# Kernel optimization log

Measured on AMD Instinct MI355X. Metric: run time of the kernel, lower is better.

## Reference

```python
import jax, jax.numpy as jnp
import numpy as np

B, S, L, D, H = 4, 4, 1024, 1024, 16  # batch, state_size, seq_len, d_model, num_heads
DEPTH = D // H
NEG = -1.0e9


def setup_inputs() -> dict:
    key = jax.random.key(0)
    ks = jax.random.split(key, 10)
    scale = 1.0 / np.sqrt(D)
    q = jax.random.normal(ks[0], (B, S, L, D), jnp.float32)
    k = jax.random.normal(ks[1], (B, S, L, D), jnp.float32)
    v = jax.random.normal(ks[2], (B, S, L, D), jnp.float32)
    mask = (jax.random.uniform(ks[3], (B, S, L, L)) < 0.1).astype(jnp.float32)
    wq = jax.random.normal(ks[4], (D, D), jnp.float32) * scale
    wk = jax.random.normal(ks[5], (D, D), jnp.float32) * scale
    wv = jax.random.normal(ks[6], (D, D), jnp.float32) * scale
    wo = jax.random.normal(ks[7], (D, D), jnp.float32) * scale
    bq = jnp.zeros((D,), jnp.float32)
    bk = jnp.zeros((D,), jnp.float32)
    bv = jnp.zeros((D,), jnp.float32)
    bo = jnp.zeros((D,), jnp.float32)
    return {"q": q, "k": k, "v": v, "mask": mask, "wq": wq, "bq": bq,
            "wk": wk, "bk": bk, "wv": wv, "bv": bv, "wo": wo, "bo": bo}


def _split_heads(x):
    # [B,S,L,D] -> [B,S,H,L,depth]
    b, s, l, _ = x.shape
    return x.reshape(b, s, l, H, DEPTH).transpose(0, 1, 3, 2, 4)


def reference(q, k, v, mask, wq, bq, wk, bk, wv, bv, wo, bo):
    qh = _split_heads(q @ wq + bq)
    kh = _split_heads(k @ wk + bk)
    vh = _split_heads(v @ wv + bv)
    # scaled dot-product attention, logits: [B,S,H,Lq,Lk]
    logits = jnp.einsum('bshqd,bshkd->bshqk', qh, kh) / jnp.sqrt(
        jnp.asarray(DEPTH, jnp.float32))
    logits = logits + mask[:, :, None, :, :] * NEG
    attn = jax.nn.softmax(logits, axis=-1)
    ctx = jnp.einsum('bshqk,bshkd->bshqd', attn, vh)
    # merge heads: [B,S,H,L,depth] -> [B,S,L,D]
    ctx = ctx.transpose(0, 1, 3, 2, 4).reshape(q.shape[0], q.shape[1], q.shape[2], D)
    out = ctx @ wo + bo
    attn_mean = attn.mean(axis=2)  # mean over heads -> [B,S,Lq,Lk]
    return out, attn_mean
```

## Files before the change

### kernel.cpp

```cpp
#include <hip/hip_runtime.h>

typedef _Float16 h16;
typedef _Float16 v8h __attribute__((ext_vector_type(8)));
typedef float    v4f __attribute__((ext_vector_type(4)));
typedef unsigned long long u64;

constexpr float SCALE = 0.125f;

#define MFMA16(a,b,c) __builtin_amdgcn_mfma_f32_16x16x32_f16((a),(b),(c),0,0,0)

__device__ __forceinline__ void gld16(const h16* g, const h16* l)
{
    __builtin_amdgcn_global_load_lds(
        (const __attribute__((address_space(1))) void*)g,
        (__attribute__((address_space(3))) void*)l, 16, 0, 0);
}

__global__ __launch_bounds__(256)
void cvt16(const float* __restrict__ x, h16* __restrict__ y)
{
    size_t i = ((size_t)blockIdx.x * 256 + threadIdx.x) * 4;
    float4 v = *(const float4*)(x + i);
    h16 o[4] = {(h16)v.x, (h16)v.y, (h16)v.z, (h16)v.w};
    *(uint2*)(y + i) = *(const uint2*)o;
}

__global__ __launch_bounds__(256)
void mkbits(const float* __restrict__ mask, u64* __restrict__ mb)
{
    size_t i = (size_t)blockIdx.x * 256 + threadIdx.x;
    float v = mask[i];
    u64 b = __ballot(v != 0.0f);
    if ((threadIdx.x & 63) == 0) mb[i >> 6] = b;
}

__global__ __launch_bounds__(256)
void wtrans(const float* __restrict__ W, h16* __restrict__ WT)
{
    __shared__ float Ts[64][65];
    const int tid = threadIdx.x;
    const int n0 = blockIdx.x * 64, k0 = blockIdx.y * 64;
    #pragma unroll
    for (int i = 0; i < 4; ++i) {
        int f = tid + i * 256; int r = f >> 4, c = (f & 15) * 4;
        float4 v = *(const float4*)(W + (size_t)(k0 + r) * 1024 + n0 + c);
        Ts[r][c] = v.x; Ts[r][c+1] = v.y; Ts[r][c+2] = v.z; Ts[r][c+3] = v.w;
    }
    __syncthreads();
    #pragma unroll
    for (int i = 0; i < 4; ++i) {
        int f = tid + i * 256; int r = f >> 4, c = (f & 15) * 4;
        h16 o[4];
        #pragma unroll
        for (int j = 0; j < 4; ++j) o[j] = (h16)Ts[c + j][r];
        *(uint2*)(WT + (size_t)(n0 + r) * 1024 + k0 + c) = *(const uint2*)o;
    }
}

__global__ __launch_bounds__(256)
void proj(const h16* __restrict__ A, const h16* __restrict__ BT,
          const float* __restrict__ bias, void* __restrict__ out, int mode)
{
    __shared__ h16 As[128 * 32];
    __shared__ h16 Bs[128 * 32];
    const int tid  = threadIdx.x;
    const int lane = tid & 63, wv = tid >> 6;
    const int quad = lane >> 4, l16 = lane & 15;
    const int m0 = blockIdx.y * 128, n0 = blockIdx.x * 128;
    const int wm = (wv & 1) * 64, wn = (wv >> 1) * 64;
    const int sr = wv * 16 + (lane >> 2);
    const int sc = (lane & 3) * 8;
    v4f acc[4][4] = {};
    for (int k0 = 0; k0 < 1024; k0 += 32) {
        #pragma unroll
        for (int i = 0; i < 2; ++i) {
            int r = i * 64 + sr;
            gld16(A  + (size_t)(m0 + r) * 1024 + k0 + sc, &As[i * 2048 + wv * 512]);
            gld16(BT + (size_t)(n0 + r) * 1024 + k0 + sc, &Bs[i * 2048 + wv * 512]);
        }
        __syncthreads();
        v8h af[4], bf[4];
        #pragma unroll
        for (int t = 0; t < 4; ++t) {
            af[t] = *(v8h*)&As[(wm + t*16 + l16) * 32 + quad * 8];
            bf[t] = *(v8h*)&Bs[(wn + t*16 + l16) * 32 + quad * 8];
        }
        #pragma unroll
        for (int mt = 0; mt < 4; ++mt)
            #pragma unroll
            for (int nt = 0; nt < 4; ++nt)
                acc[mt][nt] = MFMA16(af[mt], bf[nt], acc[mt][nt]);
        __syncthreads();
    }
    #pragma unroll
    for (int mt = 0; mt < 4; ++mt) {
        int mbase = m0 + wm + mt*16 + quad*4;
        #pragma unroll
        for (int nt = 0; nt < 4; ++nt) {
            int n = n0 + wn + nt*16 + l16;
            float bv = bias[n];
            #pragma unroll
            for (int r = 0; r < 4; ++r) {
                float y = acc[mt][nt][r] + bv;
                int mm = mbase + r;
                int bs = mm >> 10, l = mm & 1023, h = n >> 6, d = n & 63;
                if (mode <= 1)
                    ((h16*)out)[(((size_t)bs*16 + h) * 1024 + l) * 64 + d] = (h16)y;
                else if (mode == 2)
                    ((h16*)out)[(((size_t)bs*16 + h) * 64 + d) * 1024 + l] = (h16)y;
                else
                    ((float*)out)[(size_t)mm * 1024 + n] = y;
            }
        }
    }
}

__global__ __launch_bounds__(256)
void attn_ctx(const h16* __restrict__ qh, const h16* __restrict__ kh,
              const h16* __restrict__ vt, const u64* __restrict__ mbits,
              h16* __restrict__ ctx, float* __restrict__ Lst)
{
    __shared__ h16 Qs[128][72];
    __shared__ h16 Ks[64][72];
    __shared__ h16 Vs[64][72];
    __shared__ h16 Ps[128][72];
    const int tid  = threadIdx.x;
    const int lane = tid & 63, wv = tid >> 6;
    const int quad = lane >> 4, l16 = lane & 15;
    const int bsh = blockIdx.x, qb = blockIdx.y * 128;
    const int bs = bsh >> 4, h = bsh & 15;
    const int qw = wv * 32;
    #pragma unroll
    for (int i = 0; i < 4; ++i) {
        int f = tid + i * 256; int r = f >> 3, c = (f & 7) * 8;
        *(uint4*)&Qs[r][c] = *(const uint4*)(qh + ((size_t)bsh*1024 + qb + r) * 64 + c);
    }
    v4f accp[2][4] = {};
    float lsum[8] = {};
    for (int kt = 0; kt < 16; ++kt) {
        __syncthreads();
        #pragma unroll
        for (int i = 0; i < 2; ++i) {
            int f = tid + i * 256; int r = f >> 3, c = (f & 7) * 8;
            *(uint4*)&Ks[r][c] = *(const uint4*)(kh + ((size_t)bsh*1024 + kt*64 + r) * 64 + c);
            *(uint4*)&Vs[r][c] = *(const uint4*)(vt + ((size_t)bsh*64 + r) * 1024 + kt*64 + c);
        }
        __syncthreads();
        v4f s[2][4] = {};
        #pragma unroll
        for (int kc = 0; kc < 2; ++kc) {
            v8h aq[2], bk[4];
            aq[0] = *(v8h*)&Qs[qw      + l16][kc*32 + quad*8];
            aq[1] = *(v8h*)&Qs[qw + 16 + l16][kc*32 + quad*8];
            #pragma unroll
            for (int nt = 0; nt < 4; ++nt)
                bk[nt] = *(v8h*)&Ks[nt*16 + l16][kc*32 + quad*8];
            #pragma unroll
            for (int mt = 0; mt < 2; ++mt)
                #pragma unroll
                for (int nt = 0; nt < 4; ++nt)
                    s[mt][nt] = MFMA16(aq[mt], bk[nt], s[mt][nt]);
        }
        #pragma unroll
        for (int mt = 0; mt < 2; ++mt)
            #pragma unroll
            for (int r = 0; r < 4; ++r) {
                int ql = qw + mt*16 + quad*4 + r;
                u64 mrow = mbits[((size_t)bs*1024 + qb + ql) * 16 + kt];
                #pragma unroll
                for (int nt = 0; nt < 4; ++nt) {
                    int kl = nt*16 + l16;
                    float p = ((mrow >> kl) & 1ull) ? 0.0f
                                                    : __expf(s[mt][nt][r] * SCALE);
                    lsum[mt*4 + r] += p;
                    Ps[ql][kl] = (h16)p;
                }
            }
        __syncthreads();
        #pragma unroll
        for (int kc = 0; kc < 2; ++kc) {
            v8h ap[2], bv[4];
            ap[0] = *(v8h*)&Ps[qw      + l16][kc*32 + quad*8];
            ap[1] = *(v8h*)&Ps[qw + 16 + l16][kc*32 + quad*8];
            #pragma unroll
            for (int nt = 0; nt < 4; ++nt)
                bv[nt] = *(v8h*)&Vs[nt*16 + l16][kc*32 + quad*8];
            #pragma unroll
            for (int mt = 0; mt < 2; ++mt)
                #pragma unroll
                for (int nt = 0; nt < 4; ++nt)
                    accp[mt][nt] = MFMA16(ap[mt], bv[nt], accp[mt][nt]);
        }
    }
    #pragma unroll
    for (int j = 0; j < 8; ++j) {
        float v = lsum[j];
        #pragma unroll
        for (int o = 1; o < 16; o <<= 1) v += __shfl_xor(v, o);
        lsum[j] = v;
    }
    if (l16 == 0) {
        #pragma unroll
        for (int mt = 0; mt < 2; ++mt)
            #pragma unroll
            for (int r = 0; r < 4; ++r)
                Lst[(size_t)bsh*1024 + qb + qw + mt*16 + quad*4 + r] = lsum[mt*4 + r];
    }
    #pragma unroll
    for (int mt = 0; mt < 2; ++mt)
        #pragma unroll
        for (int nt = 0; nt < 4; ++nt) {
            int dep = nt*16 + l16;
            #pragma unroll
            for (int r = 0; r < 4; ++r) {
                int ql = qw + mt*16 + quad*4 + r;
                float y = accp[mt][nt][r] / lsum[mt*4 + r];
                ctx[((size_t)bs*1024 + qb + ql) * 1024 + h*64 + dep] = (h16)y;
            }
        }
}

__global__ __launch_bounds__(256)
void attn_mean_k(const h16* __restrict__ qh, const h16* __restrict__ kh,
                 const u64* __restrict__ mbits, const float* __restrict__ Lst,
                 float* __restrict__ am)
{
    __shared__ h16 Qs[128][72];
    __shared__ h16 Ks[64][72];
    const int tid  = threadIdx.x;
    const int lane = tid & 63, wv = tid >> 6;
    const int quad = lane >> 4, l16 = lane & 15;
    const int kt = blockIdx.x, qb = blockIdx.y * 128, bs = blockIdx.z;
    const int qw = wv * 32;
    u64 mrow[2][4];
    #pragma unroll
    for (int mt = 0; mt < 2; ++mt)
        #pragma unroll
        for (int r = 0; r < 4; ++r) {
            int ql = qw + mt*16 + quad*4 + r;
            mrow[mt][r] = mbits[((size_t)bs*1024 + qb + ql) * 16 + kt];
        }
    float acc[2][4][4] = {};
    for (int h = 0; h < 16; ++h) {
        const int bsh = bs * 16 + h;
        __syncthreads();
        #pragma unroll
        for (int i = 0; i < 4; ++i) {
            int f = tid + i * 256; int r = f >> 3, c = (f & 7) * 8;
            *(uint4*)&Qs[r][c] = *(const uint4*)(qh + ((size_t)bsh*1024 + qb + r) * 64 + c);
        }
        #pragma unroll
        for (int i = 0; i < 2; ++i) {
            int f = tid + i * 256; int r = f >> 3, c = (f & 7) * 8;
            *(uint4*)&Ks[r][c] = *(const uint4*)(kh + ((size_t)bsh*1024 + kt*64 + r) * 64 + c);
        }
        __syncthreads();
        v4f s[2][4] = {};
        #pragma unroll
        for (int kc = 0; kc < 2; ++kc) {
            v8h aq[2], bk[4];
            aq[0] = *(v8h*)&Qs[qw      + l16][kc*32 + quad*8];
            aq[1] = *(v8h*)&Qs[qw + 16 + l16][kc*32 + quad*8];
            #pragma unroll
            for (int nt = 0; nt < 4; ++nt)
                bk[nt] = *(v8h*)&Ks[nt*16 + l16][kc*32 + quad*8];
            #pragma unroll
            for (int mt = 0; mt < 2; ++mt)
                #pragma unroll
                for (int nt = 0; nt < 4; ++nt)
                    s[mt][nt] = MFMA16(aq[mt], bk[nt], s[mt][nt]);
        }
        float rl[8];
        #pragma unroll
        for (int mt = 0; mt < 2; ++mt)
            #pragma unroll
            for (int r = 0; r < 4; ++r)
                rl[mt*4+r] = 1.0f / Lst[(size_t)bsh*1024 + qb + qw + mt*16 + quad*4 + r];
        #pragma unroll
        for (int mt = 0; mt < 2; ++mt)
            #pragma unroll
            for (int nt = 0; nt < 4; ++nt) {
                int kl = nt*16 + l16;
                #pragma unroll
                for (int r = 0; r < 4; ++r) {
                    float e = ((mrow[mt][r] >> kl) & 1ull) ? 0.0f
                                                           : __expf(s[mt][nt][r] * SCALE);
                    acc[mt][nt][r] += e * rl[mt*4+r];
                }
            }
    }
    #pragma unroll
    for (int mt = 0; mt < 2; ++mt)
        #pragma unroll
        for (int nt = 0; nt < 4; ++nt)
            #pragma unroll
            for (int r = 0; r < 4; ++r) {
                int ql = qw + mt*16 + quad*4 + r;
                am[((size_t)bs*1024 + ql + qb) * 1024 + kt*64 + nt*16 + l16]
                    = acc[mt][nt][r] * 0.0625f;
            }
}

extern "C" void kernel_launch(void* const* d_in, const int* in_sizes, int n_in,
                              void* d_out, int out_size, void* d_ws, size_t ws_size,
                              hipStream_t stream)
{
    const float* q    = (const float*)d_in[0];
    const float* k    = (const float*)d_in[1];
    const float* v    = (const float*)d_in[2];
    const float* mask = (const float*)d_in[3];
    const float* wq   = (const float*)d_in[4];
    const float* bq   = (const float*)d_in[5];
    const float* wk   = (const float*)d_in[6];
    const float* bk   = (const float*)d_in[7];
    const float* wv   = (const float*)d_in[8];
    const float* bv   = (const float*)d_in[9];
    const float* wo   = (const float*)d_in[10];
    const float* bo   = (const float*)d_in[11];

    const size_t TEN = (size_t)16384 * 1024;
    char* w = (char*)d_ws;
    h16* qf  = (h16*)w;             w += TEN * 2;
    h16* kf  = (h16*)w;             w += TEN * 2;
    h16* vf  = (h16*)w;             w += TEN * 2;
    h16* wqT = (h16*)w;             w += (size_t)1024*1024*2;
    h16* wkT = (h16*)w;             w += (size_t)1024*1024*2;
    h16* wvT = (h16*)w;             w += (size_t)1024*1024*2;
    h16* woT = (h16*)w;             w += (size_t)1024*1024*2;
    h16* qhh = (h16*)w;             w += TEN * 2;
    h16* khh = (h16*)w;             w += TEN * 2;
    h16* vtt = (h16*)w;             w += TEN * 2;
    h16* ctx = (h16*)w;             w += TEN * 2;
    float* Lst = (float*)w;         w += (size_t)256 * 1024 * 4;
    u64* mbits = (u64*)w;

    float* out = (float*)d_out;
    float* am  = out + TEN;

    mkbits<<<65536, 256, 0, stream>>>(mask, mbits);
    cvt16<<<16384, 256, 0, stream>>>(q, qf);
    cvt16<<<16384, 256, 0, stream>>>(k, kf);
    cvt16<<<16384, 256, 0, stream>>>(v, vf);
    wtrans<<<dim3(16,16), 256, 0, stream>>>(wq, wqT);
    wtrans<<<dim3(16,16), 256, 0, stream>>>(wk, wkT);
    wtrans<<<dim3(16,16), 256, 0, stream>>>(wv, wvT);
    wtrans<<<dim3(16,16), 256, 0, stream>>>(wo, woT);
    proj<<<dim3(8,128), 256, 0, stream>>>(qf, wqT, bq, qhh, 0);
    proj<<<dim3(8,128), 256, 0, stream>>>(kf, wkT, bk, khh, 1);
    proj<<<dim3(8,128), 256, 0, stream>>>(vf, wvT, bv, vtt, 2);
    attn_ctx<<<dim3(256,8), 256, 0, stream>>>(qhh, khh, vtt, mbits, ctx, Lst);
    attn_mean_k<<<dim3(16,8,16), 256, 0, stream>>>(qhh, khh, mbits, Lst, am);
    proj<<<dim3(8,128), 256, 0, stream>>>(ctx, woT, bo, out, 3);
}
```

Measured before the change: 900.1 us.

## Fold softmax scale into Q, use exp2, MFMA row sums, register prefetch, block swizzle

```diff
diff --git a/kernel.cpp b/kernel.cpp
--- a/kernel.cpp
+++ b/kernel.cpp
@@ -5,9 +5,24 @@
 typedef float    v4f __attribute__((ext_vector_type(4)));
 typedef unsigned long long u64;
 
-constexpr float SCALE = 0.125f;
+constexpr float QPRESCALE = 0.18033688f;
 
 #define MFMA16(a,b,c) __builtin_amdgcn_mfma_f32_16x16x32_f16((a),(b),(c),0,0,0)
+
+__device__ __forceinline__ float fexp2(float x) {
+#if __has_builtin(__builtin_amdgcn_exp2f)
+    return __builtin_amdgcn_exp2f(x);
+#else
+    return __expf(x * 0.69314718056f);
+#endif
+}
+__device__ __forceinline__ float flog2(float x) {
+#if __has_builtin(__builtin_amdgcn_logf)
+    return __builtin_amdgcn_logf(x);
+#else
+    return __logf(x) * 1.44269504f;
+#endif
+}
 
 __device__ __forceinline__ void gld16(const h16* g, const h16* l)
 {
@@ -102,6 +117,7 @@
             #pragma unroll
             for (int r = 0; r < 4; ++r) {
                 float y = acc[mt][nt][r] + bv;
+                if (mode == 0) y *= QPRESCALE;
                 int mm = mbase + r;
                 int bs = mm >> 10, l = mm & 1023, h = n >> 6, d = n & 63;
                 if (mode <= 1)
@@ -115,35 +131,57 @@
     }
 }
 
-__global__ __launch_bounds__(256)
+__global__ __launch_bounds__(256, 3)
 void attn_ctx(const h16* __restrict__ qh, const h16* __restrict__ kh,
               const h16* __restrict__ vt, const u64* __restrict__ mbits,
               h16* __restrict__ ctx, float* __restrict__ Lst)
 {
-    __shared__ h16 Qs[128][72];
-    __shared__ h16 Ks[64][72];
-    __shared__ h16 Vs[64][72];
-    __shared__ h16 Ps[128][72];
+    __shared__ h16 Qs[128][68];
+    __shared__ h16 Ks[64][68];
+    __shared__ h16 Vs[64][68];
+    __shared__ h16 Ps[128][68];
     const int tid  = threadIdx.x;
     const int lane = tid & 63, wv = tid >> 6;
     const int quad = lane >> 4, l16 = lane & 15;
-    const int bsh = blockIdx.x, qb = blockIdx.y * 128;
+    const int orig = blockIdx.x + (blockIdx.y << 8);
+    const int slot = orig >> 3;
+    const int bsh  = (orig & 7) + ((slot & 31) << 3);
+    const int qb   = (slot >> 5) << 7;
     const int bs = bsh >> 4, h = bsh & 15;
     const int qw = wv * 32;
+    const int fr = tid >> 3, fc = (tid & 7) * 8;
+
+    uint4 rK0 = *(const uint4*)(kh + ((size_t)bsh*1024 + fr     ) * 64 + fc);
+    uint4 rK1 = *(const uint4*)(kh + ((size_t)bsh*1024 + fr + 32) * 64 + fc);
+    uint4 rV0 = *(const uint4*)(vt + ((size_t)bsh*64 + fr     ) * 1024 + fc);
+    uint4 rV1 = *(const uint4*)(vt + ((size_t)bsh*64 + fr + 32) * 1024 + fc);
+
     #pragma unroll
     for (int i = 0; i < 4; ++i) {
         int f = tid + i * 256; int r = f >> 3, c = (f & 7) * 8;
         *(uint4*)&Qs[r][c] = *(const uint4*)(qh + ((size_t)bsh*1024 + qb + r) * 64 + c);
     }
+    v8h bones;
+    {
+        h16 o = (l16 == 0) ? (h16)1.0f : (h16)0.0f;
+        #pragma unroll
+        for (int j = 0; j < 8; ++j) bones[j] = o;
+    }
+    const u64* mrb = mbits + ((size_t)bs*1024 + qb + qw + quad*4) * 16;
+
     v4f accp[2][4] = {};
-    float lsum[8] = {};
+    v4f accs[2] = {};
     for (int kt = 0; kt < 16; ++kt) {
         __syncthreads();
-        #pragma unroll
-        for (int i = 0; i < 2; ++i) {
-            int f = tid + i * 256; int r = f >> 3, c = (f & 7) * 8;
-            *(uint4*)&Ks[r][c] = *(const uint4*)(kh + ((size_t)bsh*1024 + kt*64 + r) * 64 + c);
-            *(uint4*)&Vs[r][c] = *(const uint4*)(vt + ((size_t)bsh*64 + r) * 1024 + kt*64 + c);
+        *(uint4*)&Ks[fr     ][fc] = rK0;
+        *(uint4*)&Ks[fr + 32][fc] = rK1;
+        *(uint4*)&Vs[fr     ][fc] = rV0;
+        *(uint4*)&Vs[fr + 32][fc] = rV1;
+        if (kt < 15) {
+            rK0 = *(const uint4*)(kh + ((size_t)bsh*1024 + (kt+1)*64 + fr     ) * 64 + fc);
+            rK1 = *(const uint4*)(kh + ((size_t)bsh*1024 + (kt+1)*64 + fr + 32) * 64 + fc);
+            rV0 = *(const uint4*)(vt + ((size_t)bsh*64 + fr     ) * 1024 + (kt+1)*64 + fc);
+            rV1 = *(const uint4*)(vt + ((size_t)bsh*64 + fr + 32) * 1024 + (kt+1)*64 + fc);
         }
         __syncthreads();
         v4f s[2][4] = {};
@@ -166,14 +204,14 @@
             #pragma unroll
             for (int r = 0; r < 4; ++r) {
                 int ql = qw + mt*16 + quad*4 + r;
-                u64 mrow = mbits[((size_t)bs*1024 + qb + ql) * 16 + kt];
+                u64 m64 = mrb[(mt*16 + r) * 16 + kt];
+                uint lo = (uint)(m64 >> l16);
+                uint hi = (uint)(m64 >> (l16 + 32));
                 #pragma unroll
                 for (int nt = 0; nt < 4; ++nt) {
-                    int kl = nt*16 + l16;
-                    float p = ((mrow >> kl) & 1ull) ? 0.0f
-                                                    : __expf(s[mt][nt][r] * SCALE);
-                    lsum[mt*4 + r] += p;
-                    Ps[ql][kl] = (h16)p;
+                    uint b = (((nt & 2) ? hi : lo) >> ((nt & 1) * 16)) & 1u;
+                    float p = b ? 0.0f : fexp2(s[mt][nt][r]);
+                    Ps[ql][nt*16 + l16] = (h16)p;
                 }
             }
         __syncthreads();
@@ -186,25 +224,30 @@
             for (int nt = 0; nt < 4; ++nt)
                 bv[nt] = *(v8h*)&Vs[nt*16 + l16][kc*32 + quad*8];
             #pragma unroll
-            for (int mt = 0; mt < 2; ++mt)
+            for (int mt = 0; mt < 2; ++mt) {
+                accs[mt] = MFMA16(ap[mt], bones, accs[mt]);
                 #pragma unroll
                 for (int nt = 0; nt < 4; ++nt)
                     accp[mt][nt] = MFMA16(ap[mt], bv[nt], accp[mt][nt]);
-        }
-    }
+            }
+        }
+    }
+    float lq[8];
+    #pragma unroll
+    for (int mt = 0; mt < 2; ++mt)
+        #pragma unroll
+        for (int r = 0; r < 4; ++r)
+            lq[mt*4 + r] = accs[mt][r];
+    if (l16 == 0) {
+        #pragma unroll
+        for (int j = 0; j < 8; ++j)
+            Lst[(size_t)bsh*1024 + qb + qw + (j >> 2)*16 + quad*4 + (j & 3)] = lq[j];
+    }
+    float rcp[8];
     #pragma unroll
     for (int j = 0; j < 8; ++j) {
-        float v = lsum[j];
-        #pragma unroll
-        for (int o = 1; o < 16; o <<= 1) v += __shfl_xor(v, o);
-        lsum[j] = v;
-    }
-    if (l16 == 0) {
-        #pragma unroll
-        for (int mt = 0; mt < 2; ++mt)
-            #pragma unroll
-            for (int r = 0; r < 4; ++r)
-                Lst[(size_t)bsh*1024 + qb + qw + mt*16 + quad*4 + r] = lsum[mt*4 + r];
+        float l = __shfl(lq[j], quad * 16);
+        rcp[j] = 1.0f / l;
     }
     #pragma unroll
     for (int mt = 0; mt < 2; ++mt)
@@ -214,7 +257,7 @@
             #pragma unroll
             for (int r = 0; r < 4; ++r) {
                 int ql = qw + mt*16 + quad*4 + r;
-                float y = accp[mt][nt][r] / lsum[mt*4 + r];
+                float y = accp[mt][nt][r] * rcp[mt*4 + r];
                 ctx[((size_t)bs*1024 + qb + ql) * 1024 + h*64 + dep] = (h16)y;
             }
         }
@@ -225,12 +268,17 @@
                  const u64* __restrict__ mbits, const float* __restrict__ Lst,
                  float* __restrict__ am)
 {
-    __shared__ h16 Qs[128][72];
-    __shared__ h16 Ks[64][72];
+    __shared__ h16 Qs[128][68];
+    __shared__ h16 Ks[64][68];
     const int tid  = threadIdx.x;
     const int lane = tid & 63, wv = tid >> 6;
     const int quad = lane >> 4, l16 = lane & 15;
-    const int kt = blockIdx.x, qb = blockIdx.y * 128, bs = blockIdx.z;
+    const int orig = blockIdx.x + (blockIdx.y << 4) + (blockIdx.z << 7);
+    const int slot = orig >> 3;
+    const int bs   = (orig & 7) + ((slot & 1) << 3);
+    const int rem  = slot >> 1;
+    const int kt   = rem & 15;
+    const int qb   = (rem >> 4) << 7;
     const int qw = wv * 32;
     u64 mrow[2][4];
     #pragma unroll
@@ -270,35 +318,34 @@
                 for (int nt = 0; nt < 4; ++nt)
                     s[mt][nt] = MFMA16(aq[mt], bk[nt], s[mt][nt]);
         }
-        float rl[8];
+        float ll[8];
         #pragma unroll
         for (int mt = 0; mt < 2; ++mt)
             #pragma unroll
             for (int r = 0; r < 4; ++r)
-                rl[mt*4+r] = 1.0f / Lst[(size_t)bsh*1024 + qb + qw + mt*16 + quad*4 + r];
+                ll[mt*4+r] = flog2(Lst[(size_t)bsh*1024 + qb + qw + mt*16 + quad*4 + r]);
         #pragma unroll
         for (int mt = 0; mt < 2; ++mt)
             #pragma unroll
+            for (int nt = 0; nt < 4; ++nt)
+                #pragma unroll
+                for (int r = 0; r < 4; ++r)
+                    acc[mt][nt][r] += fexp2(s[mt][nt][r] - ll[mt*4+r]);
+    }
+    #pragma unroll
+    for (int mt = 0; mt < 2; ++mt)
+        #pragma unroll
+        for (int r = 0; r < 4; ++r) {
+            int ql = qw + mt*16 + quad*4 + r;
+            uint lo = (uint)(mrow[mt][r] >> l16);
+            uint hi = (uint)(mrow[mt][r] >> (l16 + 32));
+            #pragma unroll
             for (int nt = 0; nt < 4; ++nt) {
-                int kl = nt*16 + l16;
-                #pragma unroll
-                for (int r = 0; r < 4; ++r) {
-                    float e = ((mrow[mt][r] >> kl) & 1ull) ? 0.0f
-                                                           : __expf(s[mt][nt][r] * SCALE);
-                    acc[mt][nt][r] += e * rl[mt*4+r];
-                }
+                uint b = (((nt & 2) ? hi : lo) >> ((nt & 1) * 16)) & 1u;
+                am[((size_t)bs*1024 + qb + ql) * 1024 + kt*64 + nt*16 + l16]
+                    = b ? 0.0f : acc[mt][nt][r] * 0.0625f;
             }
-    }
-    #pragma unroll
-    for (int mt = 0; mt < 2; ++mt)
-        #pragma unroll
-        for (int nt = 0; nt < 4; ++nt)
-            #pragma unroll
-            for (int r = 0; r < 4; ++r) {
-                int ql = qw + mt*16 + quad*4 + r;
-                am[((size_t)bs*1024 + ql + qb) * 1024 + kt*64 + nt*16 + l16]
-                    = acc[mt][nt][r] * 0.0625f;
-            }
+        }
 }
 
 extern "C" void kernel_launch(void* const* d_in, const int* in_sizes, int n_in,
```

After: 829.6 us. 7.8% less time.
